# Performance work log

Measured on AMD Instinct MI355X. Metric: run time of the kernel, lower is better.

## Reference

```python
import jax, jax.numpy as jnp
import numpy as np

B, S, H, C, T = 8, 1024, 256, 4, 12
THETA = 10000.0


def setup_inputs() -> dict:
    key = jax.random.key(0)
    ks = jax.random.split(key, 7)
    x = jax.random.normal(ks[0], (B, S, H), dtype=jnp.float32)
    token_index = jax.random.randint(ks[1], (B, S), 0, 256, dtype=jnp.int32)
    thread_id = jnp.sort(jax.random.randint(ks[2], (B, S), 0, T, dtype=jnp.int32), axis=-1)
    bound = 1.0 / np.sqrt(H)  # nn.Linear default init range
    Wq = jax.random.uniform(ks[3], (H, H * C), jnp.float32, -bound, bound)
    bq = jax.random.uniform(ks[4], (H * C,), jnp.float32, -bound, bound)
    Wk = jax.random.uniform(ks[5], (H, H * C), jnp.float32, -bound, bound)
    bk = jax.random.uniform(ks[6], (H * C,), jnp.float32, -bound, bound)
    return {"x": x, "Wq": Wq, "bq": bq, "Wk": Wk, "bk": bk,
            "token_index": token_index, "thread_id": thread_id}


def _rope(v, pos):
    # v: (B, S, C, H); pos: (B, S) signed positions
    half = v.shape[-1] // 2
    # freqs = 1 / theta^(arange(0, H, 2) / H)
    freqs = 1.0 / (THETA ** (jnp.arange(half, dtype=jnp.float32) * 2.0 / (2 * half)))
    ang = pos[..., None].astype(jnp.float32) * freqs          # (B, S, half)
    cos = jnp.cos(ang)[:, :, None, :]                          # (B, S, 1, half)
    sin = jnp.sin(ang)[:, :, None, :]
    vr = v.reshape(*v.shape[:-1], half, 2)                     # complex pairs (even, odd)
    re = vr[..., 0] * cos - vr[..., 1] * sin
    im = vr[..., 0] * sin + vr[..., 1] * cos
    return jnp.stack([re, im], axis=-1).reshape(v.shape)


def reference(x, Wq, bq, Wk, bk, token_index, thread_id):
    q = (x @ Wq + bq).reshape(B, S, C, H)
    k = (x @ Wk + bk).reshape(B, S, C, H)
    # Block sign rules of get_instance_embedding reduce to three cases per
    # token pair (m, n) with thread ids ti=thread(m), tj=thread(n):
    #   0 < ti < tj : q uses -pos, k uses +pos
    #   0 < tj < ti : q uses +pos, k uses -pos
    #   otherwise   : both use +pos
    q_pos = _rope(q, token_index)
    q_neg = _rope(q, -token_index)
    k_pos = _rope(k, token_index)
    k_neg = _rope(k, -token_index)
    l1 = jnp.einsum('bmch,bnch->bcmn', q_pos, k_pos)
    l2 = jnp.einsum('bmch,bnch->bcmn', q_neg, k_pos)
    l3 = jnp.einsum('bmch,bnch->bcmn', q_pos, k_neg)
    ti = thread_id[:, :, None]   # rows
    tj = thread_id[:, None, :]   # cols
    cond2 = ((ti > 0) & (ti < tj))[:, None, :, :]   # (B,1,S,S)
    cond3 = ((tj > 0) & (ti > tj))[:, None, :, :]
    return jnp.where(cond2, l2, jnp.where(cond3, l3, l1))  # (B, C, S, S)
```

## Files before the change

### kernel.cpp

```cpp
#include <hip/hip_runtime.h>

#define BB 8
#define SS 1024
#define HH 256
#define CC 4
#define NQ 1024

typedef unsigned short u16;
typedef unsigned int u32;
typedef __attribute__((ext_vector_type(8))) __bf16 bf16x8;
typedef __attribute__((ext_vector_type(4))) float f32x4;
typedef __attribute__((ext_vector_type(4))) u32 u32x4;
typedef __attribute__((ext_vector_type(4))) u16 u16x4;

__device__ __forceinline__ u16 f2bf(float f) {
    u32 u = __float_as_uint(f);
    u32 r = (u + 0x7FFFu + ((u >> 16) & 1u)) >> 16;
    return (u16)r;
}

__device__ __forceinline__ void gld16(const u16* g, u16* l) {
    __builtin_amdgcn_global_load_lds(
        (const __attribute__((address_space(1))) void*)g,
        (__attribute__((address_space(3))) void*)l, 16, 0, 0);
}

__device__ __forceinline__ bf16x8 ldsfrag(const u16* smem, int row, int c16) {
    const char* p = (const char*)smem + row * 128 + (((c16 ^ (row & 7)) & 7) << 4);
    return *(const bf16x8*)p;
}
__device__ __forceinline__ bf16x8 ldsfrag32(const u16* smem, int row, int c16) {
    const char* p = (const char*)smem + row * 64 + (((c16 ^ ((row >> 1) & 3)) & 3) << 4);
    return *(const bf16x8*)p;
}

#define WAITV(n) asm volatile("s_waitcnt vmcnt(" #n ")" ::: "memory")
#define WAITLG() asm volatile("s_waitcnt lgkmcnt(0)" ::: "memory")

__global__ void __launch_bounds__(256) k0_prep(
    const float4* __restrict__ x4, u16x4* __restrict__ xbf4,
    const float* __restrict__ Wq, const float* __restrict__ Wk,
    u16* __restrict__ Wt, float2* __restrict__ trig) {
    __shared__ u16 tl[64][65];
    int b = blockIdx.x;
    if (b < 2048) {
        int i = b * 256 + threadIdx.x;
        float4 v = x4[i];
        u16x4 o = {f2bf(v.x), f2bf(v.y), f2bf(v.z), f2bf(v.w)};
        xbf4[i] = o;
    } else if (b < 2176) {
        int idx = b - 2048;
        int nb = (idx & 31) * 64, kb = (idx >> 5) * 64;
        int c = threadIdx.x & 63;
#pragma unroll
        for (int r = threadIdx.x >> 6; r < 64; r += 4) {
            int k = kb + r, n = nb + c;
            float v = (n < NQ) ? Wq[k * NQ + n] : Wk[k * NQ + (n - NQ)];
            tl[c][r] = f2bf(v);
        }
        __syncthreads();
#pragma unroll
        for (int r = threadIdx.x >> 6; r < 64; r += 4) {
            Wt[(size_t)(nb + r) * HH + kb + c] = tl[r][c];
        }
    } else {
        int i = (b - 2176) * 256 + threadIdx.x;
        int pos = i >> 7, f = i & 127;
        float freq = __expf(-(float)f * 0.07195578515529633f);
        float ang = (float)pos * freq;
        float s, c;
        sincosf(ang, &s, &c);
        trig[i] = make_float2(c, s);
    }
}

#define STAGE2(dst, srcbase, roff, kc)                                          \
    _Pragma("unroll") for (int i_ = 0; i_ < 2; ++i_) {                          \
        int r_ = ww * 16 + i_ * 8 + (l >> 3);                                   \
        int c16_ = (l & 7) ^ (r_ & 7);                                          \
        gld16((srcbase) + (size_t)((roff) + r_) * HH + (kc) * 64 + c16_ * 8,    \
              (dst) + (ww * 16 + i_ * 8) * 64);                                 \
    }
#define STAGE32(dst, srcbase, roff, kc) do {                                    \
        int r_ = (threadIdx.x >> 2);                                            \
        int sl_ = (threadIdx.x & 3) ^ ((r_ >> 1) & 3);                          \
        gld16((srcbase) + (size_t)((roff) + r_) * HH + (kc) * 32 + sl_ * 8,     \
              (dst) + ww * 512);                                                \
    } while (0)

__global__ void __launch_bounds__(512, 2) k1_proj(
    const u16* __restrict__ xbf, const u16* __restrict__ Wt,
    const float* __restrict__ bq, const float* __restrict__ bk,
    const int* __restrict__ tok, const float2* __restrict__ trig,
    u16* __restrict__ qpos, u16* __restrict__ qneg,
    u16* __restrict__ kpos, u16* __restrict__ kneg) {
    int h = blockIdx.x;
    int logical = (h & 7) * 128 + (h >> 3);
    int m0 = (logical >> 4) * 128, n0 = (logical & 15) * 128;
    int ww = threadIdx.x >> 6, l = threadIdx.x & 63;
    int wr = ww >> 1, wc = ww & 1;

    __shared__ u16 sm[32768];
    u16* Ab[2] = {sm, sm + 16384};
    u16* Bb[2] = {sm + 8192, sm + 24576};

    f32x4 acc[2][4] = {};
    STAGE2(Ab[0], xbf, m0, 0)
    STAGE2(Bb[0], Wt, n0, 0)
    STAGE2(Ab[1], xbf, m0, 1)
    STAGE2(Bb[1], Wt, n0, 1)
    WAITV(4);
    __builtin_amdgcn_s_barrier();
#pragma unroll
    for (int kc = 0; kc < 4; ++kc) {
        const u16* As = Ab[kc & 1];
        const u16* Bs = Bb[kc & 1];
        __builtin_amdgcn_s_setprio(1);
#pragma unroll
        for (int ks = 0; ks < 2; ++ks) {
            int c16 = (l >> 4) + ks * 4;
            bf16x8 af[2], bfr[4];
#pragma unroll
            for (int mi = 0; mi < 2; ++mi) af[mi] = ldsfrag(As, wr * 32 + mi * 16 + (l & 15), c16);
#pragma unroll
            for (int ns = 0; ns < 4; ++ns) bfr[ns] = ldsfrag(Bs, wc * 64 + ns * 16 + (l & 15), c16);
#pragma unroll
            for (int mi = 0; mi < 2; ++mi)
#pragma unroll
                for (int ns = 0; ns < 4; ++ns)
                    acc[mi][ns] = __builtin_amdgcn_mfma_f32_16x16x32_bf16(af[mi], bfr[ns], acc[mi][ns], 0, 0, 0);
        }
        __builtin_amdgcn_s_setprio(0);
        if (kc < 3) {
            WAITLG();
            __builtin_amdgcn_s_barrier();
            if (kc < 2) {
                STAGE2(Ab[kc & 1], xbf, m0, kc + 2)
                STAGE2(Bb[kc & 1], Wt, n0, kc + 2)
                WAITV(4);
            } else {
                WAITV(0);
            }
            __builtin_amdgcn_s_barrier();
        }
    }

#pragma unroll
    for (int mi = 0; mi < 2; ++mi)
#pragma unroll
        for (int ns = 0; ns < 4; ++ns) {
            int n = n0 + wc * 64 + ns * 16 + (l & 15);
            bool isq = n < NQ;
            int nc = n & (NQ - 1);
            float bias = isq ? bq[nc] : bk[nc];
            int c = nc >> 8, hh = nc & 255, fi = hh >> 1;
#pragma unroll
            for (int r = 0; r < 4; ++r) {
                int m = m0 + wr * 32 + mi * 16 + (l >> 4) * 4 + r;
                float val = acc[mi][ns][r] + bias;
                float other = __shfl_xor(val, 1);
                int pos = tok[m];
                float2 cs = trig[pos * 128 + fi];
                float rp, rn;
                if ((l & 1) == 0) {
                    rp = val * cs.x - other * cs.y;
                    rn = val * cs.x + other * cs.y;
                } else {
                    rp = other * cs.y + val * cs.x;
                    rn = -other * cs.y + val * cs.x;
                }
                int b = m >> 10, s = m & 1023;
                size_t oidx = ((size_t)((b << 2) | c) * SS + s) * HH + hh;
                if (isq) {
                    qpos[oidx] = f2bf(rp);
                    qneg[oidx] = f2bf(rn);
                } else {
                    kpos[oidx] = f2bf(rp);
                    kneg[oidx] = f2bf(rn);
                }
            }
        }
}

__global__ void __launch_bounds__(512, 2) k2_gemm(
    const u16* __restrict__ qpos, const u16* __restrict__ qneg,
    const u16* __restrict__ kpos, const u16* __restrict__ kneg,
    const int* __restrict__ thread_id, float* __restrict__ out) {
    int h = blockIdx.x;
    int logical = (h & 7) * 256 + (h >> 3);
    int bc = logical >> 6;
    int t = logical & 63;
    int m0 = (t >> 3) * 128, n0 = (t & 7) * 128;
    const int* tb = thread_id + (bc >> 2) * SS;
    int ww = threadIdx.x >> 6, l = threadIdx.x & 63;
    int wr = ww >> 1, wc = ww & 1;
    int ti0 = tb[m0], ti1 = tb[m0 + 127], tj0 = tb[n0], tj1 = tb[n0 + 127];
    bool pure2 = (ti0 > 0) & (ti1 < tj0);
    bool pure3 = (tj0 > 0) & (ti0 > tj1);
    bool pure1 = (ti1 == 0) | (tj1 == 0) | ((ti0 == ti1) & (tj0 == tj1) & (ti0 == tj0));
    size_t base = (size_t)bc * (SS * HH);
    float* ob = out + (size_t)bc * ((size_t)SS * SS);
    int ar0 = m0 + wr * 32;
    int nb0 = n0 + wc * 64;

    __shared__ u16 sm[32768];

    if (pure1 | pure2 | pure3) {
        const u16* q = (pure2 ? qneg : qpos) + base;
        const u16* k = (pure3 ? kneg : kpos) + base;
        u16* Ab[2] = {sm, sm + 16384};
        u16* Bb[2] = {sm + 8192, sm + 24576};

        f32x4 acc[2][4] = {};
        STAGE2(Ab[0], q, m0, 0)
        STAGE2(Bb[0], k, n0, 0)
        STAGE2(Ab[1], q, m0, 1)
        STAGE2(Bb[1], k, n0, 1)
        WAITV(4);
        __builtin_amdgcn_s_barrier();
#pragma unroll
        for (int kc = 0; kc < 4; ++kc) {
            const u16* As = Ab[kc & 1];
            const u16* Bs = Bb[kc & 1];
            __builtin_amdgcn_s_setprio(1);
#pragma unroll
            for (int ks = 0; ks < 2; ++ks) {
                int c16 = (l >> 4) + ks * 4;
                bf16x8 af[2], bfr[4];
#pragma unroll
                for (int mi = 0; mi < 2; ++mi) af[mi] = ldsfrag(As, wr * 32 + mi * 16 + (l & 15), c16);
#pragma unroll
                for (int ns = 0; ns < 4; ++ns) bfr[ns] = ldsfrag(Bs, wc * 64 + ns * 16 + (l & 15), c16);
#pragma unroll
                for (int mi = 0; mi < 2; ++mi)
#pragma unroll
                    for (int ns = 0; ns < 4; ++ns)
                        acc[mi][ns] = __builtin_amdgcn_mfma_f32_16x16x32_bf16(af[mi], bfr[ns], acc[mi][ns], 0, 0, 0);
            }
            __builtin_amdgcn_s_setprio(0);
            if (kc < 3) {
                WAITLG();
                __builtin_amdgcn_s_barrier();
                if (kc < 2) {
                    STAGE2(Ab[kc & 1], q, m0, kc + 2)
                    STAGE2(Bb[kc & 1], k, n0, kc + 2)
                    WAITV(4);
                } else {
                    WAITV(0);
                }
                __builtin_amdgcn_s_barrier();
            }
        }

#pragma unroll
        for (int mi = 0; mi < 2; ++mi)
#pragma unroll
            for (int ns = 0; ns < 4; ++ns)
#pragma unroll
                for (int r = 0; r < 4; ++r) {
                    int m = ar0 + mi * 16 + (l >> 4) * 4 + r;
                    int n = nb0 + ns * 16 + (l & 15);
                    __builtin_nontemporal_store(acc[mi][ns][r], &ob[(size_t)m * SS + n]);
                }
    } else {
        const u16* qp = qpos + base;
        const u16* qn = qneg + base;
        const u16* kp = kpos + base;
        const u16* kn = kneg + base;
        u16* bufb[2] = {sm, sm + 16384};

        int bamin = ti0 > 1 ? ti0 : 1;
        int bcmin = tj0 > 1 ? tj0 : 1;
        bool B2 = (ti1 > 0) && (tj1 > bamin);
        bool B3 = (tj1 > 0) && (ti1 > bcmin);

        int fa[2], fb[2], fc[4], fd[4];
#pragma unroll
        for (int mi = 0; mi < 2; ++mi) {
            fa[mi] = tb[ar0 + mi * 16];
            fb[mi] = tb[ar0 + mi * 16 + 15];
        }
#pragma unroll
        for (int ns = 0; ns < 4; ++ns) {
            fc[ns] = tb[nb0 + ns * 16];
            fd[ns] = tb[nb0 + ns * 16 + 15];
        }
        u32 msk1 = 0, msk2 = 0, msk3 = 0;
#pragma unroll
        for (int mi = 0; mi < 2; ++mi)
#pragma unroll
            for (int ns = 0; ns < 4; ++ns) {
                u32 bit = 1u << (mi * 4 + ns);
                if ((fa[mi] == 0) | (fc[ns] == 0) | ((fa[mi] <= fd[ns]) & (fc[ns] <= fb[mi]))) msk1 |= bit;
                int amin = fa[mi] > 1 ? fa[mi] : 1;
                if ((fb[mi] > 0) & (fd[ns] > amin)) msk2 |= bit;
                int cmin = fc[ns] > 1 ? fc[ns] : 1;
                if ((fd[ns] > 0) & (fb[mi] > cmin)) msk3 |= bit;
            }
        msk1 = __builtin_amdgcn_readfirstlane(msk1);
        msk2 = __builtin_amdgcn_readfirstlane(msk2);
        msk3 = __builtin_amdgcn_readfirstlane(msk3);

#define MSTAGE(bi, kc) do {                                \
        STAGE32(bufb[bi], qp, m0, kc);                     \
        if (B2) STAGE32(bufb[bi] + 4096, qn, m0, kc);      \
        STAGE32(bufb[bi] + 8192, kp, n0, kc);              \
        if (B3) STAGE32(bufb[bi] + 12288, kn, n0, kc);     \
    } while (0)
#define WAITN() do {                                       \
        if (B2 & B3) { WAITV(4); }                         \
        else if (B2 | B3) { WAITV(3); }                    \
        else { WAITV(2); }                                 \
    } while (0)

        f32x4 a1[2][4] = {}, a2[2][4] = {}, a3[2][4] = {};
        MSTAGE(0, 0);
        MSTAGE(1, 1);
        WAITN();
        __builtin_amdgcn_s_barrier();
#pragma unroll
        for (int kc = 0; kc < 8; ++kc) {
            const u16* bqp = bufb[kc & 1];
            const u16* bqn = bqp + 4096;
            const u16* bkp = bqp + 8192;
            const u16* bkn = bqp + 12288;
            int c16 = l >> 4;
            bf16x8 qpF[2], qnF[2], kpF[4], knF[4];
            __builtin_amdgcn_s_setprio(1);
#pragma unroll
            for (int mi = 0; mi < 2; ++mi) {
                int rr = wr * 32 + mi * 16 + (l & 15);
                qpF[mi] = ldsfrag32(bqp, rr, c16);
                if (msk2) qnF[mi] = ldsfrag32(bqn, rr, c16);
            }
#pragma unroll
            for (int ns = 0; ns < 4; ++ns) {
                int rn = wc * 64 + ns * 16 + (l & 15);
                kpF[ns] = ldsfrag32(bkp, rn, c16);
                if (msk3) knF[ns] = ldsfrag32(bkn, rn, c16);
            }
#pragma unroll
            for (int mi = 0; mi < 2; ++mi)
#pragma unroll
                for (int ns = 0; ns < 4; ++ns) {
                    u32 bit = 1u << (mi * 4 + ns);
                    if (msk1 & bit)
                        a1[mi][ns] = __builtin_amdgcn_mfma_f32_16x16x32_bf16(qpF[mi], kpF[ns], a1[mi][ns], 0, 0, 0);
                    if (msk2 & bit)
                        a2[mi][ns] = __builtin_amdgcn_mfma_f32_16x16x32_bf16(qnF[mi], kpF[ns], a2[mi][ns], 0, 0, 0);
                    if (msk3 & bit)
                        a3[mi][ns] = __builtin_amdgcn_mfma_f32_16x16x32_bf16(qpF[mi], knF[ns], a3[mi][ns], 0, 0, 0);
                }
            __builtin_amdgcn_s_setprio(0);
            if (kc < 7) {
                WAITLG();
                __builtin_amdgcn_s_barrier();
                if (kc < 6) {
                    MSTAGE(kc & 1, kc + 2);
                    WAITN();
                } else {
                    WAITV(0);
                }
                __builtin_amdgcn_s_barrier();
            }
        }
#undef MSTAGE
#undef WAITN

        int tj[4], ti_[2][4];
#pragma unroll
        for (int ns = 0; ns < 4; ++ns) tj[ns] = tb[nb0 + ns * 16 + (l & 15)];
#pragma unroll
        for (int mi = 0; mi < 2; ++mi)
#pragma unroll
            for (int r = 0; r < 4; ++r) ti_[mi][r] = tb[ar0 + mi * 16 + (l >> 4) * 4 + r];

#pragma unroll
        for (int mi = 0; mi < 2; ++mi)
#pragma unroll
            for (int ns = 0; ns < 4; ++ns)
#pragma unroll
                for (int r = 0; r < 4; ++r) {
                    int m = ar0 + mi * 16 + (l >> 4) * 4 + r;
                    int n = nb0 + ns * 16 + (l & 15);
                    int ti = ti_[mi][r], tjj = tj[ns];
                    float v = (ti > 0 && ti < tjj) ? a2[mi][ns][r]
                             : ((tjj > 0 && ti > tjj) ? a3[mi][ns][r] : a1[mi][ns][r]);
                    __builtin_nontemporal_store(v, &ob[(size_t)m * SS + n]);
                }
    }
}

extern "C" void kernel_launch(void* const* d_in, const int* in_sizes, int n_in,
                              void* d_out, int out_size, void* d_ws, size_t ws_size,
                              hipStream_t stream) {
    const float* x  = (const float*)d_in[0];
    const float* Wq = (const float*)d_in[1];
    const float* bq = (const float*)d_in[2];
    const float* Wk = (const float*)d_in[3];
    const float* bk = (const float*)d_in[4];
    const int* tok  = (const int*)d_in[5];
    const int* tid  = (const int*)d_in[6];
    float* out = (float*)d_out;

    char* ws = (char*)d_ws;
    const size_t MB = 1u << 20;
    u16* qpos = (u16*)(ws);
    u16* qneg = (u16*)(ws + 16 * MB);
    u16* kpos = (u16*)(ws + 32 * MB);
    u16* kneg = (u16*)(ws + 48 * MB);
    u16* xbf  = (u16*)(ws + 64 * MB);
    u16* Wt   = (u16*)(ws + 68 * MB);
    float2* trig = (float2*)(ws + 69 * MB);

    k0_prep<<<2304, 256, 0, stream>>>((const float4*)x, (u16x4*)xbf, Wq, Wk, Wt, trig);
    k1_proj<<<1024, 512, 0, stream>>>(xbf, Wt, bq, bk, tok, trig, qpos, qneg, kpos, kneg);
    k2_gemm<<<2048, 512, 0, stream>>>(qpos, qneg, kpos, kneg, tid, out);
}
```

Measured before the change: 110.2 us.

## Switch GEMM K-loop to 32-wide chunks with triple-buffered LDS pipeline

Both the projection GEMM and the pure-case score GEMM now stage 32-element K chunks into three rotating LDS buffers instead of 64-element chunks into two. The loop runs eight K steps with two loads in flight ahead of compute, and LDS per block drops from 64KB to 48KB. The intent is deeper prefetch and lower LDS footprint, which could allow more resident blocks. The cost is twice as many barriers and waitcnt points per tile and fewer MFMAs between synchronisations.

```diff
diff --git a/kernel.cpp b/kernel.cpp
--- a/kernel.cpp
+++ b/kernel.cpp
@@ -25,10 +25,6 @@
         (__attribute__((address_space(3))) void*)l, 16, 0, 0);
 }
 
-__device__ __forceinline__ bf16x8 ldsfrag(const u16* smem, int row, int c16) {
-    const char* p = (const char*)smem + row * 128 + (((c16 ^ (row & 7)) & 7) << 4);
-    return *(const bf16x8*)p;
-}
 __device__ __forceinline__ bf16x8 ldsfrag32(const u16* smem, int row, int c16) {
     const char* p = (const char*)smem + row * 64 + (((c16 ^ ((row >> 1) & 3)) & 3) << 4);
     return *(const bf16x8*)p;
@@ -74,13 +70,6 @@
     }
 }
 
-#define STAGE2(dst, srcbase, roff, kc)                                          \
-    _Pragma("unroll") for (int i_ = 0; i_ < 2; ++i_) {                          \
-        int r_ = ww * 16 + i_ * 8 + (l >> 3);                                   \
-        int c16_ = (l & 7) ^ (r_ & 7);                                          \
-        gld16((srcbase) + (size_t)((roff) + r_) * HH + (kc) * 64 + c16_ * 8,    \
-              (dst) + (ww * 16 + i_ * 8) * 64);                                 \
-    }
 #define STAGE32(dst, srcbase, roff, kc) do {                                    \
         int r_ = (threadIdx.x >> 2);                                            \
         int sl_ = (threadIdx.x & 3) ^ ((r_ >> 1) & 3);                          \
@@ -100,44 +89,41 @@
     int ww = threadIdx.x >> 6, l = threadIdx.x & 63;
     int wr = ww >> 1, wc = ww & 1;
 
-    __shared__ u16 sm[32768];
-    u16* Ab[2] = {sm, sm + 16384};
-    u16* Bb[2] = {sm + 8192, sm + 24576};
+    __shared__ u16 sm[24576];
+    u16* bA[3] = {sm, sm + 8192, sm + 16384};
 
     f32x4 acc[2][4] = {};
-    STAGE2(Ab[0], xbf, m0, 0)
-    STAGE2(Bb[0], Wt, n0, 0)
-    STAGE2(Ab[1], xbf, m0, 1)
-    STAGE2(Bb[1], Wt, n0, 1)
+    STAGE32(bA[0], xbf, m0, 0); STAGE32(bA[0] + 4096, Wt, n0, 0);
+    STAGE32(bA[1], xbf, m0, 1); STAGE32(bA[1] + 4096, Wt, n0, 1);
+    STAGE32(bA[2], xbf, m0, 2); STAGE32(bA[2] + 4096, Wt, n0, 2);
     WAITV(4);
     __builtin_amdgcn_s_barrier();
 #pragma unroll
-    for (int kc = 0; kc < 4; ++kc) {
-        const u16* As = Ab[kc & 1];
-        const u16* Bs = Bb[kc & 1];
+    for (int kc = 0; kc < 8; ++kc) {
+        const u16* As = bA[kc % 3];
+        const u16* Bs = As + 4096;
+        int c16 = l >> 4;
+        bf16x8 af[2], bfr[4];
         __builtin_amdgcn_s_setprio(1);
 #pragma unroll
-        for (int ks = 0; ks < 2; ++ks) {
-            int c16 = (l >> 4) + ks * 4;
-            bf16x8 af[2], bfr[4];
-#pragma unroll
-            for (int mi = 0; mi < 2; ++mi) af[mi] = ldsfrag(As, wr * 32 + mi * 16 + (l & 15), c16);
-#pragma unroll
-            for (int ns = 0; ns < 4; ++ns) bfr[ns] = ldsfrag(Bs, wc * 64 + ns * 16 + (l & 15), c16);
-#pragma unroll
-            for (int mi = 0; mi < 2; ++mi)
-#pragma unroll
-                for (int ns = 0; ns < 4; ++ns)
-                    acc[mi][ns] = __builtin_amdgcn_mfma_f32_16x16x32_bf16(af[mi], bfr[ns], acc[mi][ns], 0, 0, 0);
-        }
+        for (int mi = 0; mi < 2; ++mi) af[mi] = ldsfrag32(As, wr * 32 + mi * 16 + (l & 15), c16);
+#pragma unroll
+        for (int ns = 0; ns < 4; ++ns) bfr[ns] = ldsfrag32(Bs, wc * 64 + ns * 16 + (l & 15), c16);
+#pragma unroll
+        for (int mi = 0; mi < 2; ++mi)
+#pragma unroll
+            for (int ns = 0; ns < 4; ++ns)
+                acc[mi][ns] = __builtin_amdgcn_mfma_f32_16x16x32_bf16(af[mi], bfr[ns], acc[mi][ns], 0, 0, 0);
         __builtin_amdgcn_s_setprio(0);
-        if (kc < 3) {
+        if (kc < 7) {
             WAITLG();
             __builtin_amdgcn_s_barrier();
-            if (kc < 2) {
-                STAGE2(Ab[kc & 1], xbf, m0, kc + 2)
-                STAGE2(Bb[kc & 1], Wt, n0, kc + 2)
+            if (kc < 5) {
+                STAGE32(bA[kc % 3], xbf, m0, kc + 3);
+                STAGE32(bA[kc % 3] + 4096, Wt, n0, kc + 3);
                 WAITV(4);
+            } else if (kc == 5) {
+                WAITV(2);
             } else {
                 WAITV(0);
             }
@@ -208,43 +194,40 @@
     if (pure1 | pure2 | pure3) {
         const u16* q = (pure2 ? qneg : qpos) + base;
         const u16* k = (pure3 ? kneg : kpos) + base;
-        u16* Ab[2] = {sm, sm + 16384};
-        u16* Bb[2] = {sm + 8192, sm + 24576};
+        u16* bA[3] = {sm, sm + 8192, sm + 16384};
 
         f32x4 acc[2][4] = {};
-        STAGE2(Ab[0], q, m0, 0)
-        STAGE2(Bb[0], k, n0, 0)
-        STAGE2(Ab[1], q, m0, 1)
-        STAGE2(Bb[1], k, n0, 1)
+        STAGE32(bA[0], q, m0, 0); STAGE32(bA[0] + 4096, k, n0, 0);
+        STAGE32(bA[1], q, m0, 1); STAGE32(bA[1] + 4096, k, n0, 1);
+        STAGE32(bA[2], q, m0, 2); STAGE32(bA[2] + 4096, k, n0, 2);
         WAITV(4);
         __builtin_amdgcn_s_barrier();
 #pragma unroll
-        for (int kc = 0; kc < 4; ++kc) {
-            const u16* As = Ab[kc & 1];
-            const u16* Bs = Bb[kc & 1];
+        for (int kc = 0; kc < 8; ++kc) {
+            const u16* As = bA[kc % 3];
+            const u16* Bs = As + 4096;
+            int c16 = l >> 4;
+            bf16x8 af[2], bfr[4];
             __builtin_amdgcn_s_setprio(1);
 #pragma unroll
-            for (int ks = 0; ks < 2; ++ks) {
-                int c16 = (l >> 4) + ks * 4;
-                bf16x8 af[2], bfr[4];
-#pragma unroll
-                for (int mi = 0; mi < 2; ++mi) af[mi] = ldsfrag(As, wr * 32 + mi * 16 + (l & 15), c16);
-#pragma unroll
-                for (int ns = 0; ns < 4; ++ns) bfr[ns] = ldsfrag(Bs, wc * 64 + ns * 16 + (l & 15), c16);
-#pragma unroll
-                for (int mi = 0; mi < 2; ++mi)
-#pragma unroll
-                    for (int ns = 0; ns < 4; ++ns)
-                        acc[mi][ns] = __builtin_amdgcn_mfma_f32_16x16x32_bf16(af[mi], bfr[ns], acc[mi][ns], 0, 0, 0);
-            }
+            for (int mi = 0; mi < 2; ++mi) af[mi] = ldsfrag32(As, wr * 32 + mi * 16 + (l & 15), c16);
+#pragma unroll
+            for (int ns = 0; ns < 4; ++ns) bfr[ns] = ldsfrag32(Bs, wc * 64 + ns * 16 + (l & 15), c16);
+#pragma unroll
+            for (int mi = 0; mi < 2; ++mi)
+#pragma unroll
+                for (int ns = 0; ns < 4; ++ns)
+                    acc[mi][ns] = __builtin_amdgcn_mfma_f32_16x16x32_bf16(af[mi], bfr[ns], acc[mi][ns], 0, 0, 0);
             __builtin_amdgcn_s_setprio(0);
-            if (kc < 3) {
+            if (kc < 7) {
                 WAITLG();
                 __builtin_amdgcn_s_barrier();
-                if (kc < 2) {
-                    STAGE2(Ab[kc & 1], q, m0, kc + 2)
-                    STAGE2(Bb[kc & 1], k, n0, kc + 2)
+                if (kc < 5) {
+                    STAGE32(bA[kc % 3], q, m0, kc + 3);
+                    STAGE32(bA[kc % 3] + 4096, k, n0, kc + 3);
                     WAITV(4);
+                } else if (kc == 5) {
+                    WAITV(2);
                 } else {
                     WAITV(0);
                 }
```

Result: no change. 111.4 us, median of 2 (+1.1%).
